# Optimization experiments

Measured on AMD Instinct MI355X. Metric: run time of the kernel, lower is better.

Reference implementation:

```python
import jax, jax.numpy as jnp
import numpy as np

D, H, O, NEXP, NA = 128, 256, 128, 8, 5  # na = max(1, int(8*0.7)) = 5
T = float(np.e)  # gate temperature
N_TOKENS = 131072


def ternary_quantize(w):
    # per-expert-matrix threshold: alpha = mean(|W|) over each [out,in] matrix
    alpha = jnp.mean(jnp.abs(w), axis=(-2, -1), keepdims=True)
    return jnp.sign(w) * (jnp.abs(w) > 0.5 * alpha).astype(w.dtype)


def setup_inputs() -> dict:
    key = jax.random.key(0)
    ks = jax.random.split(key, 7)
    x = jax.random.normal(ks[0], (N_TOKENS, D), dtype=jnp.float32)
    # expert params stacked over expert dim e (nn.Linear layout: [out, in])
    w1 = jax.random.normal(ks[1], (NEXP, H, D), dtype=jnp.float32) * 0.05
    b1 = jax.random.normal(ks[2], (NEXP, H), dtype=jnp.float32) * 0.05
    w2 = jax.random.normal(ks[3], (NEXP, O, H), dtype=jnp.float32) * 0.05
    b2 = jax.random.normal(ks[4], (NEXP, O), dtype=jnp.float32) * 0.05
    wg = jax.random.normal(ks[5], (NEXP, D), dtype=jnp.float32) * 0.05
    bg = jax.random.normal(ks[6], (NEXP,), dtype=jnp.float32) * 0.05
    return {"x": x, "w1": w1, "b1": b1, "w2": w2, "b2": b2, "wg": wg, "bg": bg}


def reference(x, w1, b1, w2, b2, wg, bg):
    # Ternary-quantize expert weights on the fly (TW.forward); dropout in eval mode (identity).
    w1q = ternary_quantize(w1)
    w2q = ternary_quantize(w2)
    # all-expert dense MLP: x [t,d] -> hidden [t,e,h] -> eo [t,e,o]
    hid = jax.nn.relu(jnp.einsum('td,ehd->teh', x, w1q) + b1[None, :, :])
    eo = jnp.einsum('teh,eoh->teo', hid, w2q) + b2[None, :, :]
    # BG gate: tempered softmax, top-k mask, renormalize
    p = jax.nn.softmax((x @ wg.T + bg) / T, axis=-1)          # [t,e]
    _, idx = jax.lax.top_k(p, NA)                             # [t,na]
    m = jnp.sum(jax.nn.one_hot(idx, NEXP, dtype=p.dtype), axis=-2)  # [t,e] 0/1 mask
    w = p * m
    w = w / (jnp.sum(w, axis=-1, keepdims=True) + 1e-8)
    return jnp.einsum('te,teo->to', w, eo)
```

## Files before the change

kernel.cpp:

```cpp
#include <hip/hip_runtime.h>
#include <hip/hip_bf16.h>

typedef unsigned int u32;
typedef unsigned char u8;
typedef unsigned short u16;
using f32x4  = __attribute__((ext_vector_type(4))) float;
using f32x16 = __attribute__((ext_vector_type(16))) float;
using u32x4  = __attribute__((ext_vector_type(4))) u32;
using s16x8  = __attribute__((ext_vector_type(8))) short;

#define DEV static __device__ __forceinline__

DEV u32 pk2(float a, float b) {
  u16 lo = __builtin_bit_cast(u16, __float2bfloat16(a));
  u16 hi = __builtin_bit_cast(u16, __float2bfloat16(b));
  return (u32)lo | ((u32)hi << 16);
}

DEV f32x16 MFMA32(u32x4 a, u32x4 b, f32x16 c) {
  return __builtin_amdgcn_mfma_f32_32x32x16_bf16(
      __builtin_bit_cast(s16x8, a), __builtin_bit_cast(s16x8, b), c, 0, 0, 0);
}

DEV void pl32swap(u32& a, u32& b) {
  asm volatile("v_permlane32_swap_b32 %0, %1" : "+v"(a), "+v"(b));
}

typedef const __attribute__((address_space(1))) u32 gu32;
typedef __attribute__((address_space(3))) u32 lu32;

DEV void load_lds16(const void* g, void* l) {
  __builtin_amdgcn_global_load_lds((gu32*)g, (lu32*)l, 16, 0, 0);
}

DEV u16 tq1(float v, float thr) {
  return (fabsf(v) > thr) ? (v > 0.f ? (u16)0x3F80 : (u16)0xBF80) : (u16)0;
}
DEV u32 tq2(float a, float b, float thr) {
  return (u32)tq1(a, thr) | ((u32)tq1(b, thr) << 16);
}

__global__ void k1_img_gate(const float* __restrict__ w1,
                            const float* __restrict__ w2,
                            char* __restrict__ img, const float* __restrict__ x,
                            const float* __restrict__ wg,
                            const float* __restrict__ bg, float* __restrict__ gw,
                            u8* __restrict__ maskA, u32* __restrict__ hist) {
  const int tid = threadIdx.x;
  if (blockIdx.x < 256) {
    const int b = blockIdx.x;
    const float* wsrc = (b < 128) ? (w1 + (size_t)(b >> 4) * 32768)
                                  : (w2 + (size_t)((b - 128) >> 4) * 32768);
    float s = 0.f;
    const float4* wv4 = (const float4*)wsrc;
    #pragma unroll
    for (int j = 0; j < 32; ++j) {
      float4 v = wv4[tid + j * 256];
      s += fabsf(v.x) + fabsf(v.y) + fabsf(v.z) + fabsf(v.w);
    }
    #pragma unroll
    for (int off = 32; off >= 1; off >>= 1) s += __shfl_down(s, off, 64);
    __shared__ float ws4[4];
    if ((tid & 63) == 0) ws4[tid >> 6] = s;
    __syncthreads();
    const float thr =
        0.5f * (ws4[0] + ws4[1] + ws4[2] + ws4[3]) * (1.f / 32768.f);

    int gid = b * 256 + tid;
    int l = gid & 63;
    int col = l & 31, hi = l >> 5;
    const float* src;
    char* dst;
    if (gid < 32768) {
      int ks = (gid >> 6) & 7;
      int n  = gid >> 9;
      int e  = n >> 3, ht = n & 7;
      int h  = ht * 32 + col;
      int k0 = ks * 16 + hi * 8;
      src = w1 + (size_t)e * 32768 + h * 128 + k0;
      dst = img + (size_t)n * 16384 + ks * 1024 + l * 16;
    } else {
      int id = gid - 32768;
      int sl = (id >> 6) & 7;
      int n  = id >> 9;
      int e  = n >> 3, c = n & 7;
      int ks2 = sl >> 2, ot = sl & 3;
      int o  = ot * 32 + col;
      int k0 = c * 32 + ks2 * 16 + hi * 8;
      src = w2 + (size_t)e * 32768 + o * 256 + k0;
      dst = img + (size_t)n * 16384 + 8192 + sl * 1024 + l * 16;
    }
    float4 v0 = *(const float4*)src;
    float4 v1 = *(const float4*)(src + 4);
    *(uint4*)dst = make_uint4(tq2(v0.x, v0.y, thr), tq2(v0.z, v0.w, thr),
                              tq2(v1.x, v1.y, thr), tq2(v1.z, v1.w, thr));
    return;
  }
  __shared__ float s_wg[1024];
  __shared__ float s_bg[8];
  __shared__ u32 lh[256];
  ((float4*)s_wg)[tid] = ((const float4*)wg)[tid];
  if (tid < 8) s_bg[tid] = bg[tid];
  lh[tid] = 0;
  __syncthreads();

  int t = (blockIdx.x - 256) * 256 + tid;
  const float4* xr = (const float4*)(x + (size_t)t * 128);
  float lg[8];
  #pragma unroll
  for (int e = 0; e < 8; ++e) lg[e] = s_bg[e];
  #pragma unroll
  for (int c = 0; c < 4; ++c) {
    #pragma unroll
    for (int ii = 0; ii < 8; ++ii) {
      int i = c * 8 + ii;
      float4 xv = xr[i];
      #pragma unroll
      for (int e = 0; e < 8; ++e) {
        f32x4 wv = *(const f32x4*)(s_wg + e * 128 + i * 4);
        lg[e] += xv.x * wv.x + xv.y * wv.y + xv.z * wv.z + xv.w * wv.w;
      }
    }
  }
  const float invT = 0.36787944117144233f;
  #pragma unroll
  for (int e = 0; e < 8; ++e) lg[e] *= invT;
  float mx = lg[0];
  #pragma unroll
  for (int e = 1; e < 8; ++e) mx = fmaxf(mx, lg[e]);
  float p[8], den = 0.f;
  #pragma unroll
  for (int e = 0; e < 8; ++e) { p[e] = __expf(lg[e] - mx); den += p[e]; }
  float inv = 1.f / den;
  #pragma unroll
  for (int e = 0; e < 8; ++e) p[e] *= inv;
  float gsel[8], wsum = 0.f;
  u32 m = 0;
  #pragma unroll
  for (int e = 0; e < 8; ++e) {
    int rank = 0;
    #pragma unroll
    for (int e2 = 0; e2 < 8; ++e2)
      rank += (p[e2] > p[e]) || (p[e2] == p[e] && e2 < e);
    bool sel = rank < 5;
    if (sel) m |= 1u << e;
    gsel[e] = sel ? p[e] : 0.f;
    wsum += gsel[e];
  }
  float r = 1.f / (wsum + 1e-8f);
  float* gwp = gw + (size_t)t * 8;
  *(f32x4*)gwp       = (f32x4){gsel[0] * r, gsel[1] * r, gsel[2] * r, gsel[3] * r};
  *(f32x4*)(gwp + 4) = (f32x4){gsel[4] * r, gsel[5] * r, gsel[6] * r, gsel[7] * r};
  maskA[t] = (u8)m;
  __syncthreads();
  atomicAdd(&lh[m], 1u);
  __syncthreads();
  if (lh[tid]) atomicAdd(&hist[tid << 5], lh[tid]);
}

__global__ void k2_scatter(const u32* __restrict__ hist,
                           const u8* __restrict__ maskA, u32* __restrict__ cur2,
                           u32* __restrict__ perm, u32* __restrict__ order,
                           u32* __restrict__ umask) {
  const int t = threadIdx.x;
  if (blockIdx.x < 512) {
    __shared__ u32 s[256], lh[256], lb[256];
    u32 h = hist[t << 5];
    s[t] = h;
    lh[t] = 0;
    __syncthreads();
    #pragma unroll
    for (int o = 1; o < 256; o <<= 1) {
      u32 v = (t >= o) ? s[t - o] : 0u;
      __syncthreads();
      s[t] += v;
      __syncthreads();
    }
    const u32 pbase = s[t] - h;
    int tkn = blockIdx.x * 256 + t;
    u32 m = maskA[tkn];
    u32 r = atomicAdd(&lh[m], 1u);
    __syncthreads();
    if (lh[t]) lb[t] = pbase + atomicAdd(&cur2[t << 5], lh[t]);
    __syncthreads();
    perm[lb[m] + r] = (u32)tkn;
    return;
  }
  __shared__ u32 sh[256], sA[256], spfx[256];
  __shared__ u32 bcnt[4], bcur[4], boff[4];
  __shared__ u32 L[512];
  u32 h = hist[t << 5];
  sh[t] = h;
  sA[t] = h;
  if (t < 4) { bcnt[t] = 0; bcur[t] = 0; }
  __syncthreads();
  #pragma unroll
  for (int o = 1; o < 256; o <<= 1) {
    u32 v = (t >= o) ? sA[t - o] : 0u;
    __syncthreads();
    sA[t] += v;
    __syncthreads();
  }
  spfx[t] = sA[t] - h;
  __syncthreads();
  int c[2];
  int mb[2] = {t, t + 256};
  #pragma unroll
  for (int k = 0; k < 2; ++k) {
    u32 start = (u32)mb[k] * 256u, end = start + 256u;
    u32 un = 0;
    for (int m = 0; m < 256; ++m) {
      u32 p0 = spfx[m];
      if (sh[m] && p0 < end && p0 + sh[m] > start) un |= (u32)m;
    }
    umask[mb[k]] = un;
    c[k] = (int)__popc(un);
    atomicAdd(&bcnt[8 - c[k]], 1);
  }
  __syncthreads();
  if (t == 0) {
    boff[0] = 0;
    boff[1] = bcnt[0];
    boff[2] = bcnt[0] + bcnt[1];
    boff[3] = bcnt[0] + bcnt[1] + bcnt[2];
  }
  __syncthreads();
  #pragma unroll
  for (int k = 0; k < 2; ++k) {
    int q = 8 - c[k];
    u32 pos = boff[q] + atomicAdd(&bcur[q], 1);
    L[pos] = (u32)mb[k];
  }
  __syncthreads();
  order[2 * t]     = L[t];
  order[2 * t + 1] = L[511 - t];
}

#define B1_OFF 65536
#define G_OFF  73728
#define SMEM_BYTES 81920

__global__ __launch_bounds__(256, 2) void moe_main(
    const float* __restrict__ x, const float* __restrict__ b1g,
    const float* __restrict__ b2g, const char* __restrict__ img,
    const u32* __restrict__ perm, const float* __restrict__ gw,
    const u32* __restrict__ order, const u32* __restrict__ umask,
    float* __restrict__ out) {
  extern __shared__ char smem[];
  float* s_b1 = (float*)(smem + B1_OFF);
  float* s_g  = (float*)(smem + G_OFF);
  const int tid = threadIdx.x;
  const int w = tid >> 6, l = tid & 63;
  const int col = l & 31, hi = l >> 5;
  const int bid = (int)order[blockIdx.x];
  const int base = bid * 256;
  const u32 loff = (u32)(l * 16);

  const u32 bmask = __builtin_amdgcn_readfirstlane(umask[bid]);
  u32 elist = 0;
  int cnt = 0;
  #pragma unroll
  for (int e = 0; e < 8; ++e)
    if ((bmask >> e) & 1) { elist |= (u32)e << (4 * cnt); ++cnt; }
  elist = __builtin_amdgcn_readfirstlane(elist);
  const int iters = __builtin_amdgcn_readfirstlane(cnt * 4);

  auto stage_pair = [&](int P, int slot) {
    const char* src = img + (size_t)P * 32768 + w * 8192 + loff;
    char* dst = smem + slot * 32768 + w * 8192;
    #pragma unroll
    for (int i = 0; i < 8; ++i)
      load_lds16(src + i * 1024, dst + i * 1024);
  };

  stage_pair((elist & 7) * 4, 0);

  u32x4 xf[2][8];
  {
    const u32 ptg = perm[base + tid];
    f32x4 gA = *(const f32x4*)(gw + (size_t)ptg * 8);
    f32x4 gB = *(const f32x4*)(gw + (size_t)ptg * 8 + 4);
    s_g[0 * 256 + tid] = gA.x; s_g[1 * 256 + tid] = gA.y;
    s_g[2 * 256 + tid] = gA.z; s_g[3 * 256 + tid] = gA.w;
    s_g[4 * 256 + tid] = gB.x; s_g[5 * 256 + tid] = gB.y;
    s_g[6 * 256 + tid] = gB.z; s_g[7 * 256 + tid] = gB.w;
    const float4* s = (const float4*)b1g;
    float4* d = (float4*)s_b1;
    d[tid] = s[tid];
    d[tid + 256] = s[tid + 256];

    #pragma unroll
    for (int tt = 0; tt < 2; ++tt) {
      const u32 pt = perm[base + w * 64 + tt * 32 + col];
      #pragma unroll
      for (int ks = 0; ks < 8; ++ks) {
        const float* xp = x + (size_t)pt * 128 + ks * 16 + hi * 8;
        float4 v0 = *(const float4*)xp;
        float4 v1 = *(const float4*)(xp + 4);
        xf[tt][ks] = (u32x4){pk2(v0.x, v0.y), pk2(v0.z, v0.w),
                             pk2(v1.x, v1.y), pk2(v1.z, v1.w)};
      }
    }
  }
  __syncthreads();

  f32x16 acc2[4][2];
  {
    u32x4 gf[2];
    #pragma unroll
    for (int tt = 0; tt < 2; ++tt) {
      u32x4 v = (u32x4){0u, 0u, 0u, 0u};
      if (hi == 0) {
        int t = w * 64 + tt * 32 + col;
        v = (u32x4){pk2(s_g[0 * 256 + t], s_g[1 * 256 + t]),
                    pk2(s_g[2 * 256 + t], s_g[3 * 256 + t]),
                    pk2(s_g[4 * 256 + t], s_g[5 * 256 + t]),
                    pk2(s_g[6 * 256 + t], s_g[7 * 256 + t])};
      }
      gf[tt] = v;
    }
    #pragma unroll
    for (int ot = 0; ot < 4; ++ot) {
      u32x4 af = (u32x4){0u, 0u, 0u, 0u};
      if (hi == 0) {
        int o = ot * 32 + col;
        af = (u32x4){pk2(b2g[0 * 128 + o], b2g[1 * 128 + o]),
                     pk2(b2g[2 * 128 + o], b2g[3 * 128 + o]),
                     pk2(b2g[4 * 128 + o], b2g[5 * 128 + o]),
                     pk2(b2g[6 * 128 + o], b2g[7 * 128 + o])};
      }
      f32x16 z{};
      #pragma unroll
      for (int tt = 0; tt < 2; ++tt) acc2[ot][tt] = MFMA32(af, gf[tt], z);
    }
  }

  auto chunk = [&](const char* cb, int e, int ht, float g0, float g1) {
    f32x16 a1_0{}, a1_1{};
    __builtin_amdgcn_s_setprio(1);
    #pragma unroll
    for (int ks = 0; ks < 8; ++ks) {
      u32x4 f = *(const u32x4*)(cb + ks * 1024 + loff);
      a1_0 = MFMA32(f, xf[0][ks], a1_0);
      a1_1 = MFMA32(f, xf[1][ks], a1_1);
    }
    __builtin_amdgcn_s_setprio(0);

    const float* b1b = s_b1 + e * 256 + ht * 32 + hi * 4;
    u32x4 hf[2][2];
    #pragma unroll
    for (int tt = 0; tt < 2; ++tt) {
      const f32x16& a1 = tt ? a1_1 : a1_0;
      const float g = tt ? g1 : g0;
      u32 u[8];
      #pragma unroll
      for (int rg = 0; rg < 4; ++rg) {
        f32x4 bb = *(const f32x4*)(b1b + rg * 8);
        float h0 = fmaxf(a1[rg * 4 + 0] + bb.x, 0.f) * g;
        float h1 = fmaxf(a1[rg * 4 + 1] + bb.y, 0.f) * g;
        float h2 = fmaxf(a1[rg * 4 + 2] + bb.z, 0.f) * g;
        float h3 = fmaxf(a1[rg * 4 + 3] + bb.w, 0.f) * g;
        u[rg * 2 + 0] = pk2(h0, h1);
        u[rg * 2 + 1] = pk2(h2, h3);
      }
      pl32swap(u[0], u[2]);
      pl32swap(u[1], u[3]);
      pl32swap(u[4], u[6]);
      pl32swap(u[5], u[7]);
      hf[0][tt] = (u32x4){u[0], u[1], u[2], u[3]};
      hf[1][tt] = (u32x4){u[4], u[5], u[6], u[7]};
    }

    __builtin_amdgcn_s_setprio(1);
    #pragma unroll
    for (int ks2 = 0; ks2 < 2; ++ks2) {
      #pragma unroll
      for (int ot = 0; ot < 4; ++ot) {
        u32x4 af = *(const u32x4*)(cb + 8192 + (ks2 * 4 + ot) * 1024 + loff);
        acc2[ot][0] = MFMA32(af, hf[ks2][0], acc2[ot][0]);
        acc2[ot][1] = MFMA32(af, hf[ks2][1], acc2[ot][1]);
      }
    }
    __builtin_amdgcn_s_setprio(0);
  };

  #pragma unroll 1
  for (int i = 0; i < iters; ++i) {
    asm volatile("s_waitcnt vmcnt(0)" ::: "memory");
    __builtin_amdgcn_s_barrier();
    __builtin_amdgcn_sched_barrier(0);
    if (i + 1 < iters) {
      const int j = i + 1;
      const int ej = (elist >> (4 * (j >> 2))) & 7;
      stage_pair(ej * 4 + (j & 3), j & 1);
    }
    const int ei = (elist >> (4 * (i >> 2))) & 7;
    const int ht0 = (i & 3) * 2;
    const float g0 = s_g[ei * 256 + w * 64 + col];
    const float g1 = s_g[ei * 256 + w * 64 + 32 + col];
    const char* buf = smem + (i & 1) * 32768;
    chunk(buf, ei, ht0, g0, g1);
    __builtin_amdgcn_sched_barrier(0);
    chunk(buf + 16384, ei, ht0 + 1, g0, g1);
  }

  #pragma unroll
  for (int tt = 0; tt < 2; ++tt) {
    const u32 pt = perm[base + w * 64 + tt * 32 + col];
    #pragma unroll
    for (int ot = 0; ot < 4; ++ot) {
      const f32x16& a = acc2[ot][tt];
      float* op = out + (size_t)pt * 128 + ot * 32 + hi * 4;
      #pragma unroll
      for (int rg = 0; rg < 4; ++rg)
        *(f32x4*)(op + rg * 8) =
            (f32x4){a[rg * 4 + 0], a[rg * 4 + 1], a[rg * 4 + 2], a[rg * 4 + 3]};
    }
  }
}

extern "C" void kernel_launch(void* const* d_in, const int* in_sizes, int n_in,
                              void* d_out, int out_size, void* d_ws, size_t ws_size,
                              hipStream_t stream) {
  const float* x  = (const float*)d_in[0];
  const float* w1 = (const float*)d_in[1];
  const float* b1 = (const float*)d_in[2];
  const float* w2 = (const float*)d_in[3];
  const float* b2 = (const float*)d_in[4];
  const float* wg = (const float*)d_in[5];
  const float* bg = (const float*)d_in[6];
  float* out = (float*)d_out;

  int ntok = in_sizes[0] / 128;
  int nblk = ntok / 256;

  char* ws = (char*)d_ws;
  char*  img    = ws;
  u32*   hist   = (u32*)(ws + 1048576);
  u32*   cur2   = (u32*)(ws + 1081344);
  u32*   order  = (u32*)(ws + 1114112);
  u32*   umask  = (u32*)(ws + 1116160);
  u8*    maskA  = (u8*)(ws + 1118208);
  u32*   perm   = (u32*)(ws + 1249280);
  float* gw     = (float*)(ws + 1773568);
  if (ws_size < 5967872) return;

  hipMemsetAsync(hist, 0, 65536, stream);
  k1_img_gate<<<256 + nblk, 256, 0, stream>>>(w1, w2, img, x, wg, bg,
                                              gw, maskA, hist);
  k2_scatter<<<nblk + 1, 256, 0, stream>>>(hist, maskA, cur2, perm, order,
                                           umask);

  hipFuncSetAttribute(reinterpret_cast<const void*>(moe_main),
                      hipFuncAttributeMaxDynamicSharedMemorySize, SMEM_BYTES);
  moe_main<<<nblk, 256, SMEM_BYTES, stream>>>(x, b1, b2, img, perm, gw,
                                              order, umask, out);
}
```

Baseline: 162.3 us.

## Stage x tiles through LDS with coalesced loads and split gate logits across waves

```diff
diff --git a/kernel.cpp b/kernel.cpp
--- a/kernel.cpp
+++ b/kernel.cpp
@@ -96,64 +96,84 @@
                               tq2(v1.x, v1.y, thr), tq2(v1.z, v1.w, thr));
     return;
   }
+  __shared__ f32x4 s_xT[32 * 66];
   __shared__ float s_wg[1024];
   __shared__ float s_bg[8];
+  __shared__ float s_lg[64 * 9];
   __shared__ u32 lh[256];
+
   ((float4*)s_wg)[tid] = ((const float4*)wg)[tid];
   if (tid < 8) s_bg[tid] = bg[tid];
   lh[tid] = 0;
-  __syncthreads();
-
-  int t = (blockIdx.x - 256) * 256 + tid;
-  const float4* xr = (const float4*)(x + (size_t)t * 128);
-  float lg[8];
-  #pragma unroll
-  for (int e = 0; e < 8; ++e) lg[e] = s_bg[e];
-  #pragma unroll
-  for (int c = 0; c < 4; ++c) {
-    #pragma unroll
-    for (int ii = 0; ii < 8; ++ii) {
-      int i = c * 8 + ii;
-      float4 xv = xr[i];
+
+  const int tok_base = (blockIdx.x - 256) * 256;
+  const int wv = tid >> 6;
+  const int ln = tid & 63;
+
+  #pragma unroll 1
+  for (int t4 = 0; t4 < 4; ++t4) {
+    __syncthreads();
+    const float4* src = (const float4*)(x + (size_t)(tok_base + t4 * 64) * 128);
+    #pragma unroll
+    for (int k = 0; k < 8; ++k) {
+      int f = tid + k * 256;
+      int row = f >> 5, c4 = f & 31;
+      float4 v = src[f];
+      s_xT[c4 * 66 + row] = (f32x4){v.x, v.y, v.z, v.w};
+    }
+    __syncthreads();
+    {
+      const float* wr0 = s_wg + wv * 128;
+      const float* wr1 = s_wg + (wv + 4) * 128;
+      float a0 = 0.f, a1 = 0.f;
+      #pragma unroll
+      for (int i = 0; i < 32; ++i) {
+        f32x4 xv = s_xT[i * 66 + ln];
+        f32x4 w0 = *(const f32x4*)(wr0 + i * 4);
+        f32x4 w1v = *(const f32x4*)(wr1 + i * 4);
+        a0 += xv.x * w0.x + xv.y * w0.y + xv.z * w0.z + xv.w * w0.w;
+        a1 += xv.x * w1v.x + xv.y * w1v.y + xv.z * w1v.z + xv.w * w1v.w;
+      }
+      s_lg[ln * 9 + wv]     = a0 + s_bg[wv];
+      s_lg[ln * 9 + wv + 4] = a1 + s_bg[wv + 4];
+    }
+    __syncthreads();
+    if (tid < 64) {
+      int t = tok_base + t4 * 64 + tid;
+      const float invT = 0.36787944117144233f;
+      float lg[8];
+      #pragma unroll
+      for (int e = 0; e < 8; ++e) lg[e] = s_lg[tid * 9 + e] * invT;
+      float mx = lg[0];
+      #pragma unroll
+      for (int e = 1; e < 8; ++e) mx = fmaxf(mx, lg[e]);
+      float p[8], den = 0.f;
+      #pragma unroll
+      for (int e = 0; e < 8; ++e) { p[e] = __expf(lg[e] - mx); den += p[e]; }
+      float inv = 1.f / den;
+      #pragma unroll
+      for (int e = 0; e < 8; ++e) p[e] *= inv;
+      float gsel[8], wsum = 0.f;
+      u32 m = 0;
       #pragma unroll
       for (int e = 0; e < 8; ++e) {
-        f32x4 wv = *(const f32x4*)(s_wg + e * 128 + i * 4);
-        lg[e] += xv.x * wv.x + xv.y * wv.y + xv.z * wv.z + xv.w * wv.w;
-      }
-    }
-  }
-  const float invT = 0.36787944117144233f;
-  #pragma unroll
-  for (int e = 0; e < 8; ++e) lg[e] *= invT;
-  float mx = lg[0];
-  #pragma unroll
-  for (int e = 1; e < 8; ++e) mx = fmaxf(mx, lg[e]);
-  float p[8], den = 0.f;
-  #pragma unroll
-  for (int e = 0; e < 8; ++e) { p[e] = __expf(lg[e] - mx); den += p[e]; }
-  float inv = 1.f / den;
-  #pragma unroll
-  for (int e = 0; e < 8; ++e) p[e] *= inv;
-  float gsel[8], wsum = 0.f;
-  u32 m = 0;
-  #pragma unroll
-  for (int e = 0; e < 8; ++e) {
-    int rank = 0;
-    #pragma unroll
-    for (int e2 = 0; e2 < 8; ++e2)
-      rank += (p[e2] > p[e]) || (p[e2] == p[e] && e2 < e);
-    bool sel = rank < 5;
-    if (sel) m |= 1u << e;
-    gsel[e] = sel ? p[e] : 0.f;
-    wsum += gsel[e];
-  }
-  float r = 1.f / (wsum + 1e-8f);
-  float* gwp = gw + (size_t)t * 8;
-  *(f32x4*)gwp       = (f32x4){gsel[0] * r, gsel[1] * r, gsel[2] * r, gsel[3] * r};
-  *(f32x4*)(gwp + 4) = (f32x4){gsel[4] * r, gsel[5] * r, gsel[6] * r, gsel[7] * r};
-  maskA[t] = (u8)m;
-  __syncthreads();
-  atomicAdd(&lh[m], 1u);
+        int rank = 0;
+        #pragma unroll
+        for (int e2 = 0; e2 < 8; ++e2)
+          rank += (p[e2] > p[e]) || (p[e2] == p[e] && e2 < e);
+        bool sel = rank < 5;
+        if (sel) m |= 1u << e;
+        gsel[e] = sel ? p[e] : 0.f;
+        wsum += gsel[e];
+      }
+      float r = 1.f / (wsum + 1e-8f);
+      float* gwp = gw + (size_t)t * 8;
+      *(f32x4*)gwp       = (f32x4){gsel[0] * r, gsel[1] * r, gsel[2] * r, gsel[3] * r};
+      *(f32x4*)(gwp + 4) = (f32x4){gsel[4] * r, gsel[5] * r, gsel[6] * r, gsel[7] * r};
+      maskA[t] = (u8)m;
+      atomicAdd(&lh[m], 1u);
+    }
+  }
   __syncthreads();
   if (lh[tid]) atomicAdd(&hist[tid << 5], lh[tid]);
 }
```

Result: no change. 161.8 us (-0.3%).
